# Optimization experiments

Measured on AMD Instinct MI355X. Metric: run time of the kernel, lower is better.

The kernel has to match this reference:

```python
import jax, jax.numpy as jnp
import numpy as np

SHAPE = (4, 16, 16)          # (t, h, w) latent shape
E, H, L = 576, 16, 6         # embd_dim, n_head, n_layer
DK = E // H                  # head dim = 36
SEQ = int(np.prod(SHAPE))    # 1024
B = 2


def _layernorm(x, s, b):
    m = x.mean(-1, keepdims=True)
    v = ((x - m) ** 2).mean(-1, keepdims=True)
    return (x - m) * jax.lax.rsqrt(v + 1e-5) * s + b


def _masks():
    # causal lower-triangular mask and L1 distance-decay mask (FullAttention.__init__)
    causal = np.tril(np.ones((SEQ, SEQ), dtype=bool))
    grids = np.meshgrid(*[np.arange(s) for s in SHAPE], indexing='ij')
    coords = np.stack([g.ravel() for g in grids], -1)          # [SEQ, 3]
    dist = np.abs(coords[:, None, :] - coords[None, :, :]).sum(-1).astype(np.float32)
    dm = np.exp(-dist / dist[0, -1])                            # max distance = dist[0, SEQ-1]
    return jnp.asarray(causal), jnp.asarray(dm)


def setup_inputs() -> dict:
    key = jax.random.key(0)
    ks = jax.random.split(key, 12)
    f32 = jnp.float32
    std = 1.0 / np.sqrt(E)
    pe = E // 3
    d = {}
    d['x'] = jax.random.normal(ks[0], (B, *SHAPE, E), f32)
    d['sos'] = jax.random.normal(ks[1], (E,), f32) * 0.02
    d['pe0'] = jax.random.normal(ks[2], (SHAPE[0], pe), f32) * 0.01
    d['pe1'] = jax.random.normal(ks[3], (SHAPE[1], pe), f32) * 0.01
    d['pe2'] = jax.random.normal(ks[4], (SHAPE[2], pe), f32) * 0.01
    d['ln1_s'] = jnp.ones((L, E), f32); d['ln1_b'] = jnp.zeros((L, E), f32)
    d['wq'] = jax.random.normal(ks[5], (L, E, E), f32) * std
    d['wk'] = jax.random.normal(ks[6], (L, E, E), f32) * std
    d['wv'] = jax.random.normal(ks[7], (L, E, E), f32) * std
    d['wo'] = jax.random.normal(ks[8], (L, E, E), f32) * (1.0 / np.sqrt(E * L))
    d['bo'] = jnp.zeros((L, E), f32)
    d['ln2_s'] = jnp.ones((L, E), f32); d['ln2_b'] = jnp.zeros((L, E), f32)
    d['w1'] = jax.random.normal(ks[9], (L, E, 4 * E), f32) * std
    d['b1'] = jnp.zeros((L, 4 * E), f32)
    d['w2'] = jax.random.normal(ks[10], (L, 4 * E, E), f32) * (1.0 / np.sqrt(4 * E))
    d['b2'] = jnp.zeros((L, E), f32)
    return d


def _forward(x, sos, pe0, pe1, pe2, ln1_s, ln1_b, wq, wk, wv, wo, bo,
             ln2_s, ln2_b, w1, b1, w2, b2):
    b = x.shape[0]
    causal, dm = _masks()
    h = x.reshape(b, SEQ, E)
    # RightShift: prepend learned SOS token, drop last
    h = jnp.concatenate([jnp.broadcast_to(sos, (b, 1, E)), h[:, :-1]], axis=1)
    # AddBroadcastPosEmbed (dim=-1): per-axis embeddings concatenated on channels
    pos = jnp.concatenate([
        jnp.broadcast_to(pe0[:, None, None, :], (*SHAPE, E // 3)),
        jnp.broadcast_to(pe1[None, :, None, :], (*SHAPE, E // 3)),
        jnp.broadcast_to(pe2[None, None, :, :], (*SHAPE, E // 3)),
    ], axis=-1).reshape(SEQ, E)
    h = h + pos
    scale = 1.0 / np.sqrt(DK)
    for l in range(L):  # fixed small layer loop
        y = _layernorm(h, ln1_s[l], ln1_b[l])
        q = (y @ wq[l]).reshape(b, SEQ, H, DK).transpose(0, 2, 1, 3)
        k = (y @ wk[l]).reshape(b, SEQ, H, DK).transpose(0, 2, 1, 3)
        v = (y @ wv[l]).reshape(b, SEQ, H, DK).transpose(0, 2, 1, 3)
        s = jnp.einsum('bhqd,bhkd->bhqk', q, k) * scale
        s = s * dm                              # elementwise distance-decay mask
        s = jnp.where(causal, s, -jnp.inf)       # causal masked_fill
        a = jax.nn.softmax(s, axis=-1)
        o = jnp.einsum('bhqk,bhkd->bhqd', a, v)
        o = o.transpose(0, 2, 1, 3).reshape(b, SEQ, E) @ wo[l] + bo[l]
        h = h + o
        y = _layernorm(h, ln2_s[l], ln2_b[l])
        y1 = y @ w1[l] + b1[l]
        y1 = jax.nn.sigmoid(1.702 * y1) * y1     # GeLU2
        h = h + (y1 @ w2[l] + b2[l])
    return h.reshape(b, *SHAPE, E)


def reference(x, sos, pe0, pe1, pe2, ln1_s, ln1_b, wq, wk, wv, wo, bo,
              ln2_s, ln2_b, w1, b1, w2, b2):
    return _forward(x, sos, pe0, pe1, pe2, ln1_s, ln1_b, wq, wk, wv, wo, bo,
                    ln2_s, ln2_b, w1, b1, w2, b2)
```

## Files before the change

### kernel.cpp

```cpp
#include <hip/hip_runtime.h>


#define E_    576
#define SEQ_  1024
#define B_    2
#define NH_   16
#define DK_   36
#define DKP_  64
#define NL_   6
#define FF_   2304
#define ROWS_ 2048
#define PSTRIDE_ 1179648

typedef unsigned short u16;
typedef unsigned int u32;
typedef float f32x4 __attribute__((ext_vector_type(4)));
typedef __bf16 bf16x8 __attribute__((ext_vector_type(8)));
typedef __bf16 bf16x4 __attribute__((ext_vector_type(4)));

#define MFMA16(a, b, c) __builtin_amdgcn_mfma_f32_16x16x32_bf16((a), (b), (c), 0, 0, 0)

__device__ __forceinline__ float bf2f(u16 u) {
    return __uint_as_float(((unsigned)u) << 16);
}
__device__ __forceinline__ u16 f2bf(float f) {
    unsigned u = __float_as_uint(f);
    u += 0x7fffu + ((u >> 16) & 1u);
    return (u16)(u >> 16);
}
__device__ __forceinline__ float load_in(const void* p, size_t i, int isf32) {
    return isf32 ? ((const float*)p)[i] : bf2f(((const u16*)p)[i]);
}
__device__ __forceinline__ bf16x8 ldg8(const u16* p) {
    uint4 u = *(const uint4*)p;
    bf16x8 r;
    __builtin_memcpy(&r, &u, 16);
    return r;
}
__device__ __forceinline__ void gload_lds16(const u16* g, u16* l) {
    __builtin_amdgcn_global_load_lds(
        (const __attribute__((address_space(1))) unsigned int*)g,
        (__attribute__((address_space(3))) unsigned int*)l, 16, 0, 0);
}

__global__ void detect_kernel(const u16* __restrict__ x, int* __restrict__ flag)
{
    __shared__ float red[4];
    int lane = threadIdx.x & 63, wave = threadIdx.x >> 6;
    float mx = 0.f;
    for (int i = threadIdx.x; i < 4096; i += 256) {
        float v = fabsf(bf2f(x[i]));
        if (v < 3e38f) mx = fmaxf(mx, v);
    }
    for (int off = 1; off < 64; off <<= 1) mx = fmaxf(mx, __shfl_xor(mx, off));
    if (lane == 0) red[wave] = mx;
    __syncthreads();
    if (threadIdx.x == 0) {
        float m = fmaxf(fmaxf(red[0], red[1]), fmaxf(red[2], red[3]));
        *flag = (m > 1e6f) ? 1 : 0;
    }
}

__global__ __launch_bounds__(256) void repack_kernel(
    const void* __restrict__ wq, const void* __restrict__ wk,
    const void* __restrict__ wv, const void* __restrict__ wo,
    const void* __restrict__ w1, const void* __restrict__ w2,
    u16* __restrict__ wT, const int* __restrict__ flagp)
{
    __shared__ u32 tile[64 * 33];
    int isf32 = *flagp;
    int idx = blockIdx.x, l = blockIdx.z;
    const void* src;
    u16* dst;
    size_t sbase;
    int R, C, cx, ry;
    if (idx < 324) {
        int t4 = idx / 81, rem = idx - t4 * 81;
        ry = rem / 9; cx = rem % 9; R = 576; C = 576;
        src = (t4 == 0) ? wq : (t4 == 1) ? wk : (t4 == 2) ? wv : wo;
        sbase = (size_t)l * 331776;
        dst = wT + (size_t)l * 3981312 + t4 * 331776;
    } else if (idx < 648) {
        int rem = idx - 324;
        ry = rem / 36; cx = rem % 36; R = 576; C = 2304;
        src = w1; sbase = (size_t)l * 1327104;
        dst = wT + (size_t)l * 3981312 + 1327104;
    } else {
        int rem = idx - 648;
        ry = rem / 9; cx = rem % 9; R = 2304; C = 576;
        src = w2; sbase = (size_t)l * 1327104;
        dst = wT + (size_t)l * 3981312 + 2654208;
    }
    int r0 = ry * 64, c0 = cx * 64;
    int t = threadIdx.x;
    if (isf32) {
        int chunk = t & 15, row = t >> 4;
        f32x4 vf4[4];
        #pragma unroll
        for (int i = 0; i < 4; i++) {
            int rr = row + i * 16;
            size_t g = sbase + (size_t)(r0 + rr) * C + c0 + chunk * 4;
            vf4[i] = *(const f32x4*)((const float*)src + g);
        }
        #pragma unroll
        for (int i = 0; i < 4; i++) {
            int rr = row + i * 16;
            u32 lo = (u32)f2bf(vf4[i][0]) | ((u32)f2bf(vf4[i][1]) << 16);
            u32 hi = (u32)f2bf(vf4[i][2]) | ((u32)f2bf(vf4[i][3]) << 16);
            tile[rr * 33 + chunk * 2] = lo;
            tile[rr * 33 + chunk * 2 + 1] = hi;
        }
    } else {
        int c8 = t & 7, row = t >> 3;
        uint4 vq[2];
        #pragma unroll
        for (int i = 0; i < 2; i++) {
            int rr = row + i * 32;
            size_t g = sbase + (size_t)(r0 + rr) * C + c0 + c8 * 8;
            vq[i] = *(const uint4*)((const u16*)src + g);
        }
        #pragma unroll
        for (int i = 0; i < 2; i++) {
            int rr = row + i * 32;
            u32* w = &tile[rr * 33 + c8 * 4];
            w[0] = vq[i].x; w[1] = vq[i].y; w[2] = vq[i].z; w[3] = vq[i].w;
        }
    }
    __syncthreads();
    u16* tbase = dst + ((size_t)cx * (R >> 6) + ry) * 4096;
    int k8 = t & 7, nl = t >> 3;
    #pragma unroll
    for (int i = 0; i < 2; i++) {
        int nn = nl + i * 32;
        int hw = nn >> 1, sh = (nn & 1) * 16;
        u32 v[8];
        #pragma unroll
        for (int j = 0; j < 8; j++)
            v[j] = (tile[(8 * k8 + j) * 33 + hw] >> sh) & 0xffffu;
        uint4 o;
        o.x = v[0] | (v[1] << 16);
        o.y = v[2] | (v[3] << 16);
        o.z = v[4] | (v[5] << 16);
        o.w = v[6] | (v[7] << 16);
        ((uint4*)(tbase + nn * 64))[k8 ^ (nn & 7)] = o;
    }
}

__global__ void embed_kernel(
    const void* __restrict__ x, const void* __restrict__ sos,
    const void* __restrict__ pe0, const void* __restrict__ pe1,
    const void* __restrict__ pe2, float* __restrict__ h,
    const int* __restrict__ flagp)
{
    int isf32 = *flagp;
    int row = blockIdx.x;
    int e = threadIdx.x;
    int s = row & 1023;
    float v = (s == 0) ? load_in(sos, e, isf32)
                       : load_in(x, (size_t)(row - 1) * E_ + e, isf32);
    int t = s >> 8, hh = (s >> 4) & 15, ww = s & 15;
    float p = (e < 192) ? load_in(pe0, t * 192 + e, isf32)
            : (e < 384) ? load_in(pe1, hh * 192 + e - 192, isf32)
                        : load_in(pe2, ww * 192 + e - 384, isf32);
    h[(size_t)row * E_ + e] = v + p;
}

template <int NPART>
__global__ __launch_bounds__(256) void ln_kernel(
    float* __restrict__ h, u16* __restrict__ y,
    const float* __restrict__ parts,
    const void* __restrict__ sc, const void* __restrict__ bi,
    int off0, const int* __restrict__ flagp)
{
    int isf32 = *flagp;
    int lane = threadIdx.x & 63, wave = threadIdx.x >> 6;
    int row = blockIdx.x * 4 + wave;
    float* hr = h + (size_t)row * E_;
    float v[9], s = 0.f, sq = 0.f;
    #pragma unroll
    for (int j = 0; j < 9; j++) {
        int e = lane + j * 64;
        float t = hr[e];
        #pragma unroll
        for (int pk = 0; pk < NPART; pk++)
            t += parts[(size_t)pk * PSTRIDE_ + (size_t)row * E_ + e];
        if (NPART > 0) hr[e] = t;
        v[j] = t;
        s += t;
        sq += t * t;
    }
    for (int off = 1; off < 64; off <<= 1) {
        s += __shfl_xor(s, off);
        sq += __shfl_xor(sq, off);
    }
    float mean = s * (1.0f / E_);
    float var = sq * (1.0f / E_) - mean * mean;
    float r = rsqrtf(var + 1e-5f);
    #pragma unroll
    for (int j = 0; j < 9; j++) {
        int e = lane + j * 64;
        float sce = load_in(sc, off0 + e, isf32);
        float bie = load_in(bi, off0 + e, isf32);
        y[(size_t)row * E_ + e] = f2bf((v[j] - mean) * r * sce + bie);
    }
}

template <int MODE, int SPLITK>
__global__ __launch_bounds__(512) void gemm_kernel(
    const u16* __restrict__ A, const u16* __restrict__ BtBase, int K,
    const void* __restrict__ bias, int boff, float* __restrict__ pout,
    u16* __restrict__ out, u16* __restrict__ qb, u16* __restrict__ kb,
    u16* __restrict__ vtb, const int* __restrict__ flagp)
{
    __shared__ u16 lA[8192];
    __shared__ u16 lB[4096];
    int t = threadIdx.x;
    int lane = t & 63, wave = t >> 6;
    int lw = lane & 15, lq = lane >> 4;
    int wx = wave >> 1, wy = wave & 1;
    int m0 = blockIdx.x * 128, n0 = blockIdx.y * 64;
    int z = blockIdx.z / SPLITK, kz = blockIdx.z % SPLITK;
    int Ks = K / SPLITK, kbase = kz * Ks;

    const u16* Bt = BtBase + (MODE == 0 ? (size_t)z * 331776 : 0);
    int rowS = t >> 3;
    int gc = (t & 7) ^ (rowS & 7);
    const u16* gA = A + (size_t)(m0 + rowS) * K + kbase + gc * 8;
    const u16* gB = Bt + ((size_t)(n0 >> 6)) * ((size_t)K << 6)
                  + (size_t)kbase * 64 + (size_t)t * 8;
    size_t rstep = (size_t)64 * K;

    f32x4 acc[2][2];
    for (int mi = 0; mi < 2; mi++)
        for (int ni = 0; ni < 2; ni++)
            for (int r = 0; r < 4; r++) acc[mi][ni][r] = 0.f;

    for (int kc = 0; kc < Ks; kc += 64) {
        gload_lds16(gA + kc,         &lA[t * 8]);
        gload_lds16(gA + rstep + kc, &lA[4096 + t * 8]);
        gload_lds16(gB + kc * 64,    &lB[t * 8]);
        __syncthreads();
        #pragma unroll
        for (int ks = 0; ks < 2; ks++) {
            int csw = ((ks * 4 + lq) ^ (lw & 7)) * 8;
            bf16x8 bf0 = ldg8(&lB[(wy * 32 + lw) * 64 + csw]);
            bf16x8 bf1 = ldg8(&lB[(wy * 32 + 16 + lw) * 64 + csw]);
            #pragma unroll
            for (int mi = 0; mi < 2; mi++) {
                bf16x8 af = ldg8(&lA[(wx * 32 + mi * 16 + lw) * 64 + csw]);
                acc[mi][0] = MFMA16(af, bf0, acc[mi][0]);
                acc[mi][1] = MFMA16(af, bf1, acc[mi][1]);
            }
        }
        __syncthreads();
    }

    int isf32 = (MODE != 0) ? *flagp : 0;
    #pragma unroll
    for (int ni = 0; ni < 2; ni++) {
        int n = n0 + wy * 32 + ni * 16 + lw;
        float bn = 0.f;
        if (MODE == 2 || ((MODE == 1 || MODE == 3) && kz == 0))
            bn = load_in(bias, boff + n, isf32);
        #pragma unroll
        for (int mi = 0; mi < 2; mi++) {
            #pragma unroll
            for (int r = 0; r < 4; r++) {
                int m = m0 + wx * 32 + mi * 16 + lq * 4 + r;
                float v = acc[mi][ni][r];
                if (MODE == 0) {
                    int b = m >> 10, s = m & 1023;
                    int head = n / 36, d = n - head * 36;
                    size_t bh = (size_t)(b * NH_ + head);
                    if (z == 0)
                        qb[(bh * SEQ_ + s) * DKP_ + d] = f2bf(v * (1.0f / 6.0f));
                    else if (z == 1)
                        kb[(bh * SEQ_ + s) * DKP_ + d] = f2bf(v);
                    else
                        vtb[(bh * DKP_ + d) * SEQ_ + s] = f2bf(v);
                } else if (MODE == 2) {
                    float tt = v + bn;
                    out[(size_t)m * FF_ + n] = f2bf(tt / (1.0f + __expf(-1.702f * tt)));
                } else {
                    pout[(size_t)kz * PSTRIDE_ + (size_t)m * E_ + n] = v + bn;
                }
            }
        }
    }
}

__global__ __launch_bounds__(256, 4) void attn_kernel(
    const u16* __restrict__ qb, const u16* __restrict__ kb,
    const u16* __restrict__ vtb, u16* __restrict__ ob)
{
    __shared__ float sm[4][16], sl[4][16], so[4][16][52];
    int lane = threadIdx.x & 63, wave = threadIdx.x >> 6;
    int lw = lane & 15, lq = lane >> 4;
    int L = blockIdx.x;
    int bh = L & 31;
    int qt = 63 - (L >> 5);
    int head = bh & 15, b = bh >> 4;
    int q0 = qt * 16;

    const u16* qrow = qb + ((size_t)bh * SEQ_ + q0 + lw) * DKP_ + lq * 8;
    bf16x8 qf0 = ldg8(qrow);
    bf16x8 qf1 = ldg8(qrow + 32);

    int tq = q0 >> 8, hq = (q0 >> 4) & 15;
    int qg = q0 + lw;
    int wq8 = (lq & 1) * 8;
    float ew8[8];
    #pragma unroll
    for (int i = 0; i < 8; i++)
        ew8[i] = __expf((float)abs(lw - (wq8 + i)) * (-1.0f / 33.0f));

    float m_i = -1e30f, l_i = 0.f;
    f32x4 oacc[3];
    #pragma unroll
    for (int c2 = 0; c2 < 3; c2++)
        #pragma unroll
        for (int r = 0; r < 4; r++) oacc[c2][r] = 0.f;

    int kperm = (lw >> 2) * 8 + (lw & 3);
    const u16* kbh = kb + (size_t)bh * SEQ_ * DKP_;
    const u16* vbh = vtb + (size_t)bh * DKP_ * SEQ_;

    int nch = (q0 >> 6) + 1;
    for (int c = wave; c < nch; c += 4) {
        int kv0 = c * 64;
        bf16x8 kf[4][2], vf[3][2];
        #pragma unroll
        for (int kvh = 0; kvh < 4; kvh++) {
            const u16* kp = kbh +
                (size_t)(kv0 + (kvh >> 1) * 32 + (kvh & 1) * 4 + kperm) * DKP_
                + lq * 8;
            kf[kvh][0] = ldg8(kp);
            kf[kvh][1] = ldg8(kp + 32);
        }
        #pragma unroll
        for (int c2 = 0; c2 < 3; c2++) {
            const u16* vp = vbh + (size_t)(c2 * 16 + lw) * SEQ_ + kv0 + lq * 8;
            vf[c2][0] = ldg8(vp);
            vf[c2][1] = ldg8(vp + 32);
        }
        f32x4 st[4];
        #pragma unroll
        for (int kvh = 0; kvh < 4; kvh++) {
            f32x4 tt;
            #pragma unroll
            for (int r = 0; r < 4; r++) tt[r] = 0.f;
            tt = MFMA16(kf[kvh][0], qf0, tt);
            tt = MFMA16(kf[kvh][1], qf1, tt);
            st[kvh] = tt;
        }
        int tk = kv0 >> 8, hk0 = (kv0 >> 4) & 15;
        float sB[4];
        #pragma unroll
        for (int i = 0; i < 4; i++)
            sB[i] = __expf((float)(abs(tq - tk) + abs(hq - hk0 - i))
                           * (-1.0f / 33.0f));
        float fh0 = sB[lq >> 1], fh1 = sB[(lq >> 1) + 2];
        float vv[4][4];
        #pragma unroll
        for (int kvh = 0; kvh < 4; kvh++) {
            float fh = (kvh < 2) ? fh0 : fh1;
            #pragma unroll
            for (int r = 0; r < 4; r++)
                vv[kvh][r] = st[kvh][r] * (fh * ew8[(kvh & 1) * 4 + r]);
        }
        if (c == nch - 1) {
            #pragma unroll
            for (int kvh = 0; kvh < 4; kvh++) {
                int koff = kv0 + (kvh >> 1) * 32 + lq * 8 + (kvh & 1) * 4;
                #pragma unroll
                for (int r = 0; r < 4; r++)
                    if (koff + r > qg) vv[kvh][r] = -1e30f;
            }
        }
        float mloc =
            fmaxf(fmaxf(fmaxf(fmaxf(vv[0][0], vv[0][1]), fmaxf(vv[0][2], vv[0][3])),
                        fmaxf(fmaxf(vv[1][0], vv[1][1]), fmaxf(vv[1][2], vv[1][3]))),
                  fmaxf(fmaxf(fmaxf(vv[2][0], vv[2][1]), fmaxf(vv[2][2], vv[2][3])),
                        fmaxf(fmaxf(vv[3][0], vv[3][1]), fmaxf(vv[3][2], vv[3][3]))));
        mloc = fmaxf(mloc, __shfl_xor(mloc, 16));
        mloc = fmaxf(mloc, __shfl_xor(mloc, 32));
        float mn = fmaxf(m_i, mloc);
        float alpha = __expf(m_i - mn);
        m_i = mn;
        float p[4][4];
        float rs = 0.f;
        #pragma unroll
        for (int kvh = 0; kvh < 4; kvh++) {
            #pragma unroll
            for (int r = 0; r < 4; r++) {
                p[kvh][r] = __expf(vv[kvh][r] - mn);
                rs += p[kvh][r];
            }
        }
        rs += __shfl_xor(rs, 16);
        rs += __shfl_xor(rs, 32);
        l_i = l_i * alpha + rs;
        #pragma unroll
        for (int c2 = 0; c2 < 3; c2++)
            #pragma unroll
            for (int r = 0; r < 4; r++) oacc[c2][r] *= alpha;
        bf16x8 pf0, pf1;
        #pragma unroll
        for (int r = 0; r < 4; r++) {
            pf0[r]     = (__bf16)p[0][r];
            pf0[4 + r] = (__bf16)p[1][r];
            pf1[r]     = (__bf16)p[2][r];
            pf1[4 + r] = (__bf16)p[3][r];
        }
        #pragma unroll
        for (int c2 = 0; c2 < 3; c2++) {
            oacc[c2] = MFMA16(vf[c2][0], pf0, oacc[c2]);
            oacc[c2] = MFMA16(vf[c2][1], pf1, oacc[c2]);
        }
    }

    if (lq == 0) { sm[wave][lw] = m_i; sl[wave][lw] = l_i; }
    #pragma unroll
    for (int c2 = 0; c2 < 3; c2++)
        #pragma unroll
        for (int r = 0; r < 4; r++)
            so[wave][lw][c2 * 16 + lq * 4 + r] = oacc[c2][r];
    __syncthreads();
    for (int i = threadIdx.x; i < 16 * DK_; i += 256) {
        int row = i / DK_, col = i - row * DK_;
        float M = fmaxf(fmaxf(sm[0][row], sm[1][row]),
                        fmaxf(sm[2][row], sm[3][row]));
        float Lm = 0.f, O = 0.f;
        #pragma unroll
        for (int w = 0; w < 4; w++) {
            float f = __expf(sm[w][row] - M);
            Lm += f * sl[w][row];
            O += f * so[w][row][col];
        }
        ob[((size_t)b * SEQ_ + q0 + row) * E_ + head * DK_ + col] = f2bf(O / Lm);
    }
}

__global__ void out_kernel(const float* __restrict__ h,
                           const float* __restrict__ p3,
                           void* __restrict__ out,
                           const int* __restrict__ flagp)
{
    int isf32 = *flagp;
    size_t i = (size_t)blockIdx.x * blockDim.x + threadIdx.x;
    float v = h[i] + p3[i] + p3[i + PSTRIDE_] + p3[i + 2 * PSTRIDE_]
            + p3[i + 3 * PSTRIDE_];
    if (isf32) ((float*)out)[i] = v;
    else       ((u16*)out)[i] = f2bf(v);
}

extern "C" void kernel_launch(void* const* d_in, const int* in_sizes, int n_in,
                              void* d_out, int out_size, void* d_ws,
                              size_t ws_size, hipStream_t stream)
{
    const void* x    = d_in[0];
    const void* sos  = d_in[1];
    const void* pe0  = d_in[2];
    const void* pe1  = d_in[3];
    const void* pe2  = d_in[4];
    const void* ln1s = d_in[5];
    const void* ln1b = d_in[6];
    const void* wq   = d_in[7];
    const void* wk   = d_in[8];
    const void* wv   = d_in[9];
    const void* wo   = d_in[10];
    const void* bo   = d_in[11];
    const void* ln2s = d_in[12];
    const void* ln2b = d_in[13];
    const void* w1   = d_in[14];
    const void* b1   = d_in[15];
    const void* w2   = d_in[16];
    const void* b2   = d_in[17];

    char* ws = (char*)d_ws;
    u16*   qbuf  = (u16*)(ws + 0);
    u16*   kbuf  = (u16*)(ws + 4194304);
    u16*   vtbuf = (u16*)(ws + 8388608);
    float* h     = (float*)(ws + 12582912);
    u16*   y     = (u16*)(ws + 17301504);
    u16*   o     = (u16*)(ws + 19660800);
    u16*   y1    = (u16*)(ws + 22020096);
    u16*   wT    = (u16*)(ws + 31457280);
    int*   flag  = (int*)(ws + 79233024);
    float* p1    = (float*)(ws + 83886080);
    float* p3    = (float*)(ws + 100663296);

    hipMemsetAsync(ws, 0, 12582912, stream);
    detect_kernel<<<1, 256, 0, stream>>>((const u16*)x, flag);
    repack_kernel<<<dim3(972, 1, 6), 256, 0, stream>>>(
        wq, wk, wv, wo, w1, w2, wT, flag);
    embed_kernel<<<ROWS_, E_, 0, stream>>>(x, sos, pe0, pe1, pe2, h, flag);

    for (int l = 0; l < NL_; l++) {
        u16* wTl = wT + (size_t)l * 3981312;
        if (l == 0)
            ln_kernel<0><<<512, 256, 0, stream>>>(h, y, nullptr, ln1s, ln1b,
                                                  l * E_, flag);
        else
            ln_kernel<4><<<512, 256, 0, stream>>>(h, y, p3, ln1s, ln1b,
                                                  l * E_, flag);
        gemm_kernel<0, 1><<<dim3(16, 9, 3), 512, 0, stream>>>(
            y, wTl, E_, nullptr, 0, nullptr, nullptr, qbuf, kbuf, vtbuf, flag);
        attn_kernel<<<dim3(2048), 256, 0, stream>>>(qbuf, kbuf, vtbuf, o);
        gemm_kernel<1, 3><<<dim3(16, 9, 3), 512, 0, stream>>>(
            o, wTl + 995328, E_, bo, l * E_, p1, nullptr, nullptr, nullptr, nullptr, flag);
        ln_kernel<3><<<512, 256, 0, stream>>>(h, y, p1, ln2s, ln2b,
                                              l * E_, flag);
        gemm_kernel<2, 1><<<dim3(16, 36, 1), 512, 0, stream>>>(
            y, wTl + 1327104, E_, b1, l * FF_, nullptr, y1, nullptr, nullptr, nullptr, flag);
        gemm_kernel<3, 4><<<dim3(16, 9, 4), 512, 0, stream>>>(
            y1, wTl + 2654208, FF_, b2, l * E_, p3, nullptr, nullptr, nullptr, nullptr, flag);
    }
    out_kernel<<<4608, 256, 0, stream>>>(h, p3, d_out, flag);
}
```

Measured before the change: 741.5 us.

## Switch attention to 32x32x16 MFMA with 32-query tiles per block

Rewrites the attention kernel to use 32x32x16 bf16 MFMA instead of 16x16x32, so each block handles 32 query rows rather than 16 and the grid is halved. Each K/V chunk loaded per wave is now reused across twice as many queries, which cuts redundant global K/V loads and reduces cross-lane shuffles in the softmax reduction. The cost is more registers per thread (launch bounds lowered to 2 blocks per SM), fewer blocks for load balancing, and wasted MFMA work on the padded head dimension (36 of 64 columns).

```diff
diff --git a/kernel.cpp b/kernel.cpp
--- a/kernel.cpp
+++ b/kernel.cpp
@@ -15,10 +15,12 @@
 typedef unsigned short u16;
 typedef unsigned int u32;
 typedef float f32x4 __attribute__((ext_vector_type(4)));
+typedef float f32x16 __attribute__((ext_vector_type(16)));
 typedef __bf16 bf16x8 __attribute__((ext_vector_type(8)));
 typedef __bf16 bf16x4 __attribute__((ext_vector_type(4)));
 
 #define MFMA16(a, b, c) __builtin_amdgcn_mfma_f32_16x16x32_bf16((a), (b), (c), 0, 0, 0)
+#define MFMA32(a, b, c) __builtin_amdgcn_mfma_f32_32x32x16_bf16((a), (b), (c), 0, 0, 0)
 
 __device__ __forceinline__ float bf2f(u16 u) {
     return __uint_as_float(((unsigned)u) << 16);
@@ -289,144 +291,146 @@
     }
 }
 
-__global__ __launch_bounds__(256, 4) void attn_kernel(
+__global__ __launch_bounds__(256, 2) void attn_kernel(
     const u16* __restrict__ qb, const u16* __restrict__ kb,
     const u16* __restrict__ vtb, u16* __restrict__ ob)
 {
-    __shared__ float sm[4][16], sl[4][16], so[4][16][52];
+    __shared__ float sm[4][32], sl[4][32], so[4][32][37];
     int lane = threadIdx.x & 63, wave = threadIdx.x >> 6;
-    int lw = lane & 15, lq = lane >> 4;
+    int q5 = lane & 31, hi = lane >> 5, hi8 = hi * 8;
     int L = blockIdx.x;
     int bh = L & 31;
-    int qt = 63 - (L >> 5);
+    int qt = 31 - (L >> 5);
     int head = bh & 15, b = bh >> 4;
-    int q0 = qt * 16;
-
-    const u16* qrow = qb + ((size_t)bh * SEQ_ + q0 + lw) * DKP_ + lq * 8;
-    bf16x8 qf0 = ldg8(qrow);
-    bf16x8 qf1 = ldg8(qrow + 32);
-
-    int tq = q0 >> 8, hq = (q0 >> 4) & 15;
-    int qg = q0 + lw;
-    int wq8 = (lq & 1) * 8;
+    int q0 = qt * 32;
+
+    const u16* qrow = qb + ((size_t)bh * SEQ_ + q0 + q5) * DKP_ + hi8;
+    bf16x8 qf[4];
+    #pragma unroll
+    for (int d16 = 0; d16 < 4; d16++) qf[d16] = ldg8(qrow + d16 * 16);
+
+    int tq = q0 >> 8;
+    int hq = ((q0 >> 4) & 15) + (q5 >> 4);
+    int qg = q0 + q5;
+    int wq = q5 & 15;
     float ew8[8];
     #pragma unroll
-    for (int i = 0; i < 8; i++)
-        ew8[i] = __expf((float)abs(lw - (wq8 + i)) * (-1.0f / 33.0f));
+    for (int j = 0; j < 8; j++)
+        ew8[j] = __expf((float)abs(wq - (j + hi8)) * (-1.0f / 33.0f));
 
     float m_i = -1e30f, l_i = 0.f;
-    f32x4 oacc[3];
-    #pragma unroll
-    for (int c2 = 0; c2 < 3; c2++)
-        #pragma unroll
-        for (int r = 0; r < 4; r++) oacc[c2][r] = 0.f;
-
-    int kperm = (lw >> 2) * 8 + (lw & 3);
+    f32x16 oacc[2];
+    #pragma unroll
+    for (int Dt = 0; Dt < 2; Dt++)
+        #pragma unroll
+        for (int r = 0; r < 16; r++) oacc[Dt][r] = 0.f;
+
+    int kp = (q5 & ~12) | ((q5 & 4) << 1) | ((q5 & 8) >> 1);
     const u16* kbh = kb + (size_t)bh * SEQ_ * DKP_;
     const u16* vbh = vtb + (size_t)bh * DKP_ * SEQ_;
 
-    int nch = (q0 >> 6) + 1;
+    int nch = (qt >> 1) + 1;
     for (int c = wave; c < nch; c += 4) {
         int kv0 = c * 64;
-        bf16x8 kf[4][2], vf[3][2];
-        #pragma unroll
-        for (int kvh = 0; kvh < 4; kvh++) {
-            const u16* kp = kbh +
-                (size_t)(kv0 + (kvh >> 1) * 32 + (kvh & 1) * 4 + kperm) * DKP_
-                + lq * 8;
-            kf[kvh][0] = ldg8(kp);
-            kf[kvh][1] = ldg8(kp + 32);
-        }
-        #pragma unroll
-        for (int c2 = 0; c2 < 3; c2++) {
-            const u16* vp = vbh + (size_t)(c2 * 16 + lw) * SEQ_ + kv0 + lq * 8;
-            vf[c2][0] = ldg8(vp);
-            vf[c2][1] = ldg8(vp + 32);
-        }
-        f32x4 st[4];
-        #pragma unroll
-        for (int kvh = 0; kvh < 4; kvh++) {
-            f32x4 tt;
-            #pragma unroll
-            for (int r = 0; r < 4; r++) tt[r] = 0.f;
-            tt = MFMA16(kf[kvh][0], qf0, tt);
-            tt = MFMA16(kf[kvh][1], qf1, tt);
-            st[kvh] = tt;
-        }
+        bf16x8 kf[2][4], vf[2][4];
+        #pragma unroll
+        for (int T = 0; T < 2; T++) {
+            const u16* kr = kbh + (size_t)(kv0 + T * 32 + kp) * DKP_ + hi8;
+            #pragma unroll
+            for (int d16 = 0; d16 < 4; d16++) kf[T][d16] = ldg8(kr + d16 * 16);
+        }
+        #pragma unroll
+        for (int s = 0; s < 4; s++)
+            vf[0][s] = ldg8(vbh + (size_t)q5 * SEQ_ + kv0 + s * 16 + hi8);
+        f32x16 st[2];
+        #pragma unroll
+        for (int T = 0; T < 2; T++) {
+            f32x16 tt;
+            #pragma unroll
+            for (int r = 0; r < 16; r++) tt[r] = 0.f;
+            #pragma unroll
+            for (int d16 = 0; d16 < 4; d16++)
+                tt = MFMA32(kf[T][d16], qf[d16], tt);
+            st[T] = tt;
+        }
+        #pragma unroll
+        for (int s = 0; s < 4; s++)
+            vf[1][s] = ldg8(vbh + (size_t)(32 + q5) * SEQ_ + kv0 + s * 16 + hi8);
         int tk = kv0 >> 8, hk0 = (kv0 >> 4) & 15;
         float sB[4];
         #pragma unroll
         for (int i = 0; i < 4; i++)
             sB[i] = __expf((float)(abs(tq - tk) + abs(hq - hk0 - i))
                            * (-1.0f / 33.0f));
-        float fh0 = sB[lq >> 1], fh1 = sB[(lq >> 1) + 2];
-        float vv[4][4];
-        #pragma unroll
-        for (int kvh = 0; kvh < 4; kvh++) {
-            float fh = (kvh < 2) ? fh0 : fh1;
-            #pragma unroll
-            for (int r = 0; r < 4; r++)
-                vv[kvh][r] = st[kvh][r] * (fh * ew8[(kvh & 1) * 4 + r]);
-        }
+        float vv[2][16];
+        #pragma unroll
+        for (int T = 0; T < 2; T++)
+            #pragma unroll
+            for (int r = 0; r < 16; r++) {
+                int j = (r & 3) + ((r >> 2) & 1) * 4;
+                int hidx = T * 2 + ((r >> 3) & 1);
+                vv[T][r] = st[T][r] * (sB[hidx] * ew8[j]);
+            }
         if (c == nch - 1) {
             #pragma unroll
-            for (int kvh = 0; kvh < 4; kvh++) {
-                int koff = kv0 + (kvh >> 1) * 32 + lq * 8 + (kvh & 1) * 4;
+            for (int T = 0; T < 2; T++)
                 #pragma unroll
-                for (int r = 0; r < 4; r++)
-                    if (koff + r > qg) vv[kvh][r] = -1e30f;
-            }
-        }
-        float mloc =
-            fmaxf(fmaxf(fmaxf(fmaxf(vv[0][0], vv[0][1]), fmaxf(vv[0][2], vv[0][3])),
-                        fmaxf(fmaxf(vv[1][0], vv[1][1]), fmaxf(vv[1][2], vv[1][3]))),
-                  fmaxf(fmaxf(fmaxf(vv[2][0], vv[2][1]), fmaxf(vv[2][2], vv[2][3])),
-                        fmaxf(fmaxf(vv[3][0], vv[3][1]), fmaxf(vv[3][2], vv[3][3]))));
-        mloc = fmaxf(mloc, __shfl_xor(mloc, 16));
+                for (int r = 0; r < 16; r++) {
+                    int key = kv0 + T * 32 + ((r >> 3) & 1) * 16 + hi8
+                            + (r & 3) + ((r >> 2) & 1) * 4;
+                    if (key > qg) vv[T][r] = -1e30f;
+                }
+        }
+        float mloc = -1e30f;
+        #pragma unroll
+        for (int T = 0; T < 2; T++)
+            #pragma unroll
+            for (int r = 0; r < 16; r++) mloc = fmaxf(mloc, vv[T][r]);
         mloc = fmaxf(mloc, __shfl_xor(mloc, 32));
         float mn = fmaxf(m_i, mloc);
         float alpha = __expf(m_i - mn);
         m_i = mn;
-        float p[4][4];
+        float p[2][16];
         float rs = 0.f;
         #pragma unroll
-        for (int kvh = 0; kvh < 4; kvh++) {
-            #pragma unroll
-            for (int r = 0; r < 4; r++) {
-                p[kvh][r] = __expf(vv[kvh][r] - mn);
-                rs += p[kvh][r];
+        for (int T = 0; T < 2; T++)
+            #pragma unroll
+            for (int r = 0; r < 16; r++) {
+                p[T][r] = __expf(vv[T][r] - mn);
+                rs += p[T][r];
             }
-        }
-        rs += __shfl_xor(rs, 16);
         rs += __shfl_xor(rs, 32);
         l_i = l_i * alpha + rs;
         #pragma unroll
-        for (int c2 = 0; c2 < 3; c2++)
-            #pragma unroll
-            for (int r = 0; r < 4; r++) oacc[c2][r] *= alpha;
-        bf16x8 pf0, pf1;
-        #pragma unroll
-        for (int r = 0; r < 4; r++) {
-            pf0[r]     = (__bf16)p[0][r];
-            pf0[4 + r] = (__bf16)p[1][r];
-            pf1[r]     = (__bf16)p[2][r];
-            pf1[4 + r] = (__bf16)p[3][r];
-        }
-        #pragma unroll
-        for (int c2 = 0; c2 < 3; c2++) {
-            oacc[c2] = MFMA16(vf[c2][0], pf0, oacc[c2]);
-            oacc[c2] = MFMA16(vf[c2][1], pf1, oacc[c2]);
-        }
-    }
-
-    if (lq == 0) { sm[wave][lw] = m_i; sl[wave][lw] = l_i; }
-    #pragma unroll
-    for (int c2 = 0; c2 < 3; c2++)
+        for (int Dt = 0; Dt < 2; Dt++)
+            #pragma unroll
+            for (int r = 0; r < 16; r++) oacc[Dt][r] *= alpha;
+        bf16x8 pf[4];
+        #pragma unroll
+        for (int T = 0; T < 2; T++)
+            #pragma unroll
+            for (int sp = 0; sp < 2; sp++)
+                #pragma unroll
+                for (int e = 0; e < 8; e++)
+                    pf[T * 2 + sp][e] = (__bf16)p[T][sp * 8 + e];
+        #pragma unroll
+        for (int Dt = 0; Dt < 2; Dt++)
+            #pragma unroll
+            for (int s = 0; s < 4; s++)
+                oacc[Dt] = MFMA32(vf[Dt][s], pf[s], oacc[Dt]);
+    }
+
+    if (hi == 0) { sm[wave][q5] = m_i; sl[wave][q5] = l_i; }
+    #pragma unroll
+    for (int r = 0; r < 16; r++)
+        so[wave][q5][(r & 3) + 8 * (r >> 2) + 4 * hi] = oacc[0][r];
+    if (hi == 0) {
         #pragma unroll
         for (int r = 0; r < 4; r++)
-            so[wave][lw][c2 * 16 + lq * 4 + r] = oacc[c2][r];
+            so[wave][q5][32 + r] = oacc[1][r];
+    }
     __syncthreads();
-    for (int i = threadIdx.x; i < 16 * DK_; i += 256) {
+    for (int i = threadIdx.x; i < 32 * DK_; i += 256) {
         int row = i / DK_, col = i - row * DK_;
         float M = fmaxf(fmaxf(sm[0][row], sm[1][row]),
                         fmaxf(sm[2][row], sm[3][row]));
@@ -506,7 +510,7 @@
                                                   l * E_, flag);
         gemm_kernel<0, 1><<<dim3(16, 9, 3), 512, 0, stream>>>(
             y, wTl, E_, nullptr, 0, nullptr, nullptr, qbuf, kbuf, vtbuf, flag);
-        attn_kernel<<<dim3(2048), 256, 0, stream>>>(qbuf, kbuf, vtbuf, o);
+        attn_kernel<<<dim3(1024), 256, 0, stream>>>(qbuf, kbuf, vtbuf, o);
         gemm_kernel<1, 3><<<dim3(16, 9, 3), 512, 0, stream>>>(
             o, wTl + 995328, E_, bo, l * E_, p1, nullptr, nullptr, nullptr, nullptr, flag);
         ln_kernel<3><<<512, 256, 0, stream>>>(h, y, p1, ln2s, ln2b,
```

After: 701.1 us (median of 2 runs). 1.06x faster.
